# Performance work log

Hardware: AMD Instinct MI355X
Metric: run time of the kernel (lower is better)

Reference implementation:

```python
import jax, jax.numpy as jnp
import numpy as np

B, L, D, F, T = 32, 768, 256, 256, 3072
_EPS = 1e-5


def _layernorm(h, g, b):
    mu = jnp.mean(h, axis=-1, keepdims=True)
    var = jnp.var(h, axis=-1, keepdims=True)
    return (h - mu) * jax.lax.rsqrt(var + _EPS) * g + b


def _conv1d(h, w, b):
    # h: [B, L, Cin], w: [K, Cin, Cout] (HIO), padding=1 matches torch Conv1d(padding=1)
    return jax.lax.conv_general_dilated(h, w, (1,), [(1, 1)], dimension_numbers=('NHC', 'HIO', 'NHC')) + b


def setup_inputs() -> dict:
    key = jax.random.key(0)
    ks = jax.random.split(key, 6)
    return {
        'x': jax.random.normal(ks[0], (B, L, D), jnp.float32),
        'target': jax.random.randint(ks[1], (B, L), 0, 4, jnp.int32),
        'mel_max_length': T,
        'conv1_w': jax.random.normal(ks[2], (3, D, F), jnp.float32) * 0.05,
        'conv1_b': jnp.zeros((F,), jnp.float32),
        'ln1_g': jnp.ones((F,), jnp.float32),
        'ln1_b': jnp.zeros((F,), jnp.float32),
        'conv2_w': jax.random.normal(ks[3], (3, F, F), jnp.float32) * 0.05,
        'conv2_b': jnp.zeros((F,), jnp.float32),
        'ln2_g': jnp.ones((F,), jnp.float32),
        'ln2_b': jnp.zeros((F,), jnp.float32),
        'lin_w': jax.random.normal(ks[4], (F, 1), jnp.float32) * 0.05,
        'lin_b': jnp.zeros((1,), jnp.float32),
    }


def reference(x, target, mel_max_length, conv1_w, conv1_b, ln1_g, ln1_b,
              conv2_w, conv2_b, ln2_g, ln2_b, lin_w, lin_b):
    alpha = 1.0
    # DurationPredictor: conv -> relu -> LN -> conv -> relu -> LN -> linear (dropout=0)
    h = _layernorm(jax.nn.relu(_conv1d(x, conv1_w, conv1_b)), ln1_g, ln1_b)
    h = _layernorm(jax.nn.relu(_conv1d(h, conv2_w, conv2_b)), ln2_g, ln2_b)
    dp_out = (h @ lin_w + lin_b)[..., 0]                       # [B, L]
    durations = jnp.exp(dp_out) * alpha                        # [B, L] float
    # Training branch: durations come from target
    dpo = jnp.round(target.astype(jnp.float32) * alpha).astype(jnp.int32)  # [B, L]
    # LR: alignment @ x realized as cumulative-duration searchsorted + gather
    cum = jnp.cumsum(dpo, axis=1)                              # [B, L]
    t = jnp.arange(mel_max_length, dtype=jnp.int32)            # [T]
    idx = jax.vmap(lambda c: jnp.searchsorted(c, t, side='right'))(cum)  # [B, T]
    mask = (t[None, :] < cum[:, -1:]).astype(x.dtype)          # [B, T] zero past total frames
    out = jnp.take_along_axis(x, jnp.clip(idx, 0, x.shape[1] - 1)[:, :, None], axis=1)
    out = out * mask[:, :, None]                               # [B, T, D]
    return (out, dpo, durations)
```

## Files before the change

kernel.cpp:

```cpp
#include <hip/hip_runtime.h>
#include <hip/hip_bf16.h>
#include <math.h>

#define BB 32
#define LL 768
#define DD 256
#define FF 256
#define TT 3072
#define MT 32
#define OS 257

typedef __attribute__((ext_vector_type(8))) short bf16x8;
typedef __attribute__((ext_vector_type(4))) float f32x4;

__device__ inline unsigned short f2b(float f) {
    union { float f; unsigned u; } v; v.f = f;
    unsigned r = (v.u + 0x7FFF + ((v.u >> 16) & 1)) >> 16;
    return (unsigned short)r;
}

__global__ __launch_bounds__(256) void prep_w_kernel(
    const float* __restrict__ w1, const float* __restrict__ w2,
    unsigned short* __restrict__ wQ1, unsigned short* __restrict__ wQ2)
{
    const int layer = blockIdx.x / 24;
    const int s  = blockIdx.x % 24;
    const int kc = s >> 3, c8 = s & 7;
    const float* __restrict__ w = layer ? w2 : w1;
    unsigned short* __restrict__ o = (layer ? wQ2 : wQ1) + s * 8192 + threadIdx.x * 32;
    const int n = threadIdx.x;

    alignas(16) unsigned short tmp[32];
#pragma unroll
    for (int q = 0; q < 4; ++q)
#pragma unroll
        for (int j = 0; j < 8; ++j) {
            const int cin = c8 * 32 + q * 8 + j;
            tmp[q * 8 + j] = f2b(w[((size_t)(kc * 256 + cin)) * 256 + n]);
        }
#pragma unroll
    for (int i = 0; i < 4; ++i)
        *reinterpret_cast<uint4*>(o + i * 8) = *reinterpret_cast<const uint4*>(tmp + i * 8);
}

template <bool SECOND>
__global__ __launch_bounds__(256) void conv_mfma_kernel(
    const void* __restrict__ in_,
    const unsigned short* __restrict__ wQ,
    const float* __restrict__ cbias,
    const float* __restrict__ g,
    const float* __restrict__ be,
    const float* __restrict__ lin_w,
    const float* __restrict__ lin_b,
    unsigned short* __restrict__ out_h,
    float* __restrict__ out_dur)
{
    __shared__ union {
        unsigned short Af[48 * 64 * 8];
        float outs[MT * OS];
    } sm;
    __shared__ float red[4][MT][2];
    __shared__ float fin[MT][2];

    const int tid  = threadIdx.x;
    const int b    = blockIdx.x / (LL / MT);
    const int l0   = (blockIdx.x % (LL / MT)) * MT;
    const int wave = tid >> 6, lane = tid & 63;
    const int quad = lane >> 4, l16 = lane & 15;

    const int col = tid;
    const float biasv = cbias[col];
    const float gv  = g[col];
    const float bv  = be[col];
    const float lwv = SECOND ? lin_w[col] : 0.f;
    const float lbv = SECOND ? lin_b[0] : 0.f;

    for (int i = 0; i < 12; ++i) {
        const int combo = i * 4 + wave;
        const int mt = combo & 1;
        const int sc = combo >> 1;
        const int kc = sc >> 3, c8 = sc & 7;
        const int l  = l0 + mt * 16 + l16 + kc - 1;
        const int ch = c8 * 32 + quad * 8;
        bf16x8 val;
#pragma unroll
        for (int j = 0; j < 8; ++j) val[j] = 0;
        if (l >= 0 && l < LL) {
            if (!SECOND) {
                const float* p = (const float*)in_ + ((size_t)b * LL + l) * DD + ch;
                const float4 v0 = *reinterpret_cast<const float4*>(p);
                const float4 v1 = *reinterpret_cast<const float4*>(p + 4);
                val[0] = (short)f2b(v0.x); val[1] = (short)f2b(v0.y);
                val[2] = (short)f2b(v0.z); val[3] = (short)f2b(v0.w);
                val[4] = (short)f2b(v1.x); val[5] = (short)f2b(v1.y);
                val[6] = (short)f2b(v1.z); val[7] = (short)f2b(v1.w);
            } else {
                val = *reinterpret_cast<const bf16x8*>(
                    (const unsigned short*)in_ + ((size_t)b * LL + l) * DD + ch);
            }
        }
        *reinterpret_cast<bf16x8*>(&sm.Af[(combo * 64 + lane) * 8]) = val;
    }
    __syncthreads();

    const unsigned short* aptr = &sm.Af[lane * 8];
    const unsigned short* bptr = wQ + wave * 2048 + (l16 * 4 + quad) * 8;

    f32x4 acc[2][4] = {};
    bf16x8 a_c[2], b_c[4];
#pragma unroll
    for (int mt = 0; mt < 2; ++mt)
        a_c[mt] = *reinterpret_cast<const bf16x8*>(aptr + mt * 512);
#pragma unroll
    for (int nt = 0; nt < 4; ++nt)
        b_c[nt] = *reinterpret_cast<const bf16x8*>(bptr + nt * 512);

    for (int s = 0; s < 24; ++s) {
        bf16x8 a_n[2], b_n[4];
        if (s < 23) {
#pragma unroll
            for (int mt = 0; mt < 2; ++mt)
                a_n[mt] = *reinterpret_cast<const bf16x8*>(aptr + (s + 1) * 1024 + mt * 512);
#pragma unroll
            for (int nt = 0; nt < 4; ++nt)
                b_n[nt] = *reinterpret_cast<const bf16x8*>(bptr + (size_t)(s + 1) * 8192 + nt * 512);
        }
#pragma unroll
        for (int mt = 0; mt < 2; ++mt)
#pragma unroll
            for (int nt = 0; nt < 4; ++nt)
                acc[mt][nt] = __builtin_amdgcn_mfma_f32_16x16x32_bf16(
                    a_c[mt], b_c[nt], acc[mt][nt], 0, 0, 0);
        if (s < 23) {
#pragma unroll
            for (int mt = 0; mt < 2; ++mt) a_c[mt] = a_n[mt];
#pragma unroll
            for (int nt = 0; nt < 4; ++nt) b_c[nt] = b_n[nt];
        }
    }
    __syncthreads();

#pragma unroll
    for (int mt = 0; mt < 2; ++mt)
#pragma unroll
        for (int nt = 0; nt < 4; ++nt)
#pragma unroll
            for (int r = 0; r < 4; ++r)
                sm.outs[(mt * 16 + quad * 4 + r) * OS + wave * 64 + nt * 16 + l16] =
                    acc[mt][nt][r];
    __syncthreads();

    float vv[MT];
#pragma unroll
    for (int r = 0; r < MT; ++r)
        vv[r] = fmaxf(sm.outs[r * OS + col] + biasv, 0.f);

#pragma unroll
    for (int r = 0; r < MT; ++r) {
        float v = vv[r];
        float sum = v, sq = v * v;
        for (int off = 32; off > 0; off >>= 1) {
            sum += __shfl_down(sum, off, 64);
            sq  += __shfl_down(sq,  off, 64);
        }
        if (lane == 0) { red[wave][r][0] = sum; red[wave][r][1] = sq; }
    }
    __syncthreads();
    if (tid < MT) {
        const float sum = red[0][tid][0] + red[1][tid][0] + red[2][tid][0] + red[3][tid][0];
        const float sq  = red[0][tid][1] + red[1][tid][1] + red[2][tid][1] + red[3][tid][1];
        const float mu  = sum / FF;
        const float var = sq / FF - mu * mu;
        fin[tid][0] = mu;
        fin[tid][1] = rsqrtf(var + 1e-5f);
    }
    __syncthreads();

#pragma unroll
    for (int r = 0; r < MT; ++r) {
        const float v = (vv[r] - fin[r][0]) * fin[r][1] * gv + bv;
        if (!SECOND) {
            out_h[((size_t)b * LL + l0 + r) * FF + col] = f2b(v);
        } else {
            float p = v * lwv;
            for (int off = 32; off > 0; off >>= 1) p += __shfl_down(p, off, 64);
            if (lane == 0) red[wave][r][0] = p;
        }
    }
    if (SECOND) {
        __syncthreads();
        if (tid < MT) {
            const float dp = red[0][tid][0] + red[1][tid][0] + red[2][tid][0]
                           + red[3][tid][0] + lbv;
            out_dur[(size_t)b * LL + l0 + tid] = expf(dp);
        }
    }
}

__global__ __launch_bounds__(256) void scan_kernel(
    const int* __restrict__ target,
    float* __restrict__ out_dpo,
    int* __restrict__ idx_map)
{
    __shared__ int tsum[256];
    const int b = blockIdx.x, tid = threadIdx.x;

    const int l = 3 * tid;
    const int v0 = target[b * LL + l];
    const int v1 = target[b * LL + l + 1];
    const int v2 = target[b * LL + l + 2];
    out_dpo[b * LL + l]     = (float)v0;
    out_dpo[b * LL + l + 1] = (float)v1;
    out_dpo[b * LL + l + 2] = (float)v2;

    const int s0 = v0, s1 = v0 + v1, s2 = v0 + v1 + v2;
    tsum[tid] = s2;
    __syncthreads();
    for (int off = 1; off < 256; off <<= 1) {
        int x = (tid >= off) ? tsum[tid - off] : 0;
        __syncthreads();
        tsum[tid] += x;
        __syncthreads();
    }
    const int excl = tsum[tid] - s2;

    for (int t = tid; t < TT; t += 256) idx_map[b * TT + t] = -1;
    __syncthreads();

    const int c0 = excl + s0, c1 = excl + s1, c2 = excl + s2;
    for (int t = excl; t < c0 && t < TT; ++t) idx_map[b * TT + t] = l;
    for (int t = c0;   t < c1 && t < TT; ++t) idx_map[b * TT + t] = l + 1;
    for (int t = c1;   t < c2 && t < TT; ++t) idx_map[b * TT + t] = l + 2;
}

__global__ __launch_bounds__(256) void gather_kernel(
    const float* __restrict__ x,
    const int* __restrict__ idx_map,
    float* __restrict__ out)
{
    const int wv = threadIdx.x >> 6, lane = threadIdx.x & 63;
    const int row = blockIdx.x * 4 + wv;
    const int b = row / TT, t = row - b * TT;
    const int idx = idx_map[b * TT + t];
    float4 val = make_float4(0.f, 0.f, 0.f, 0.f);
    if (idx >= 0)
        val = reinterpret_cast<const float4*>(x)[(size_t)(b * LL + idx) * (DD / 4) + lane];
    reinterpret_cast<float4*>(out)[(size_t)row * (DD / 4) + lane] = val;
}

extern "C" void kernel_launch(void* const* d_in, const int* in_sizes, int n_in,
                              void* d_out, int out_size, void* d_ws, size_t ws_size,
                              hipStream_t stream)
{
    const float* x      = (const float*)d_in[0];
    const int*   target = (const int*)  d_in[1];
    const float* c1w = (const float*)d_in[3];
    const float* c1b = (const float*)d_in[4];
    const float* g1  = (const float*)d_in[5];
    const float* b1  = (const float*)d_in[6];
    const float* c2w = (const float*)d_in[7];
    const float* c2b = (const float*)d_in[8];
    const float* g2  = (const float*)d_in[9];
    const float* b2  = (const float*)d_in[10];
    const float* lw  = (const float*)d_in[11];
    const float* lb  = (const float*)d_in[12];

    float* out0    = (float*)d_out;
    float* out_dpo = out0 + (size_t)BB * TT * DD;
    float* out_dur = out_dpo + (size_t)BB * LL;

    char* ws = (char*)d_ws;
    unsigned short* wQ1 = (unsigned short*)ws;                 ws += (size_t)24 * 8192 * 2;
    unsigned short* wQ2 = (unsigned short*)ws;                 ws += (size_t)24 * 8192 * 2;
    unsigned short* h1b = (unsigned short*)ws;                 ws += (size_t)BB * LL * FF * 2;
    int* idx_map        = (int*)ws;

    prep_w_kernel<<<48, 256, 0, stream>>>(c1w, c2w, wQ1, wQ2);

    const int conv_grid = BB * (LL / MT);
    conv_mfma_kernel<false><<<conv_grid, 256, 0, stream>>>(
        x, wQ1, c1b, g1, b1, nullptr, nullptr, h1b, nullptr);
    conv_mfma_kernel<true><<<conv_grid, 256, 0, stream>>>(
        h1b, wQ2, c2b, g2, b2, lw, lb, nullptr, out_dur);

    scan_kernel<<<BB, 256, 0, stream>>>(target, out_dpo, idx_map);
    gather_kernel<<<BB * TT / 4, 256, 0, stream>>>(x, idx_map, out0);
}
```

Baseline: 235.3 us.

## Fuse both conv+LN layers into one kernel with halo recompute

Merges the two conv/ReLU/LayerNorm kernels into a single kernel per 32-row tile. Each block recomputes conv1 over a 2-row halo (48 rows) so conv2 can read h1 from shared memory, removing the global write and read of the bf16 intermediate and one launch. LayerNorm now reduces directly from MFMA accumulators via lane shuffles instead of staging through shared memory. The cost is about 50% extra conv1 MFMA work, and the B-operand prefetch double-buffering is dropped.

Result: faster. 209.0 us (-11.2%).

```diff
diff --git a/kernel.cpp b/kernel.cpp
--- a/kernel.cpp
+++ b/kernel.cpp
@@ -8,7 +8,8 @@
 #define FF 256
 #define TT 3072
 #define MT 32
-#define OS 257
+#define PAD 264
+#define A1R 50
 
 typedef __attribute__((ext_vector_type(8))) short bf16x8;
 typedef __attribute__((ext_vector_type(4))) float f32x4;
@@ -43,24 +44,22 @@
         *reinterpret_cast<uint4*>(o + i * 8) = *reinterpret_cast<const uint4*>(tmp + i * 8);
 }
 
-template <bool SECOND>
-__global__ __launch_bounds__(256) void conv_mfma_kernel(
-    const void* __restrict__ in_,
-    const unsigned short* __restrict__ wQ,
-    const float* __restrict__ cbias,
-    const float* __restrict__ g,
-    const float* __restrict__ be,
-    const float* __restrict__ lin_w,
-    const float* __restrict__ lin_b,
-    unsigned short* __restrict__ out_h,
+__global__ __launch_bounds__(256) void fused_dp_kernel(
+    const float* __restrict__ x,
+    const unsigned short* __restrict__ wQ1,
+    const unsigned short* __restrict__ wQ2,
+    const float* __restrict__ c1b, const float* __restrict__ g1, const float* __restrict__ b1,
+    const float* __restrict__ c2b, const float* __restrict__ g2, const float* __restrict__ b2,
+    const float* __restrict__ lw,  const float* __restrict__ lb,
     float* __restrict__ out_dur)
 {
     __shared__ union {
-        unsigned short Af[48 * 64 * 8];
-        float outs[MT * OS];
+        unsigned short A1[A1R * PAD];
+        unsigned short h2[34 * PAD];
     } sm;
-    __shared__ float red[4][MT][2];
-    __shared__ float fin[MT][2];
+    __shared__ float red[4][3][4][4][2];
+    __shared__ float redp[4][2][4][4];
+    __shared__ float fin[48][2];
 
     const int tid  = threadIdx.x;
     const int b    = blockIdx.x / (LL / MT);
@@ -68,132 +67,185 @@
     const int wave = tid >> 6, lane = tid & 63;
     const int quad = lane >> 4, l16 = lane & 15;
 
-    const int col = tid;
-    const float biasv = cbias[col];
-    const float gv  = g[col];
-    const float bv  = be[col];
-    const float lwv = SECOND ? lin_w[col] : 0.f;
-    const float lbv = SECOND ? lin_b[0] : 0.f;
-
-    for (int i = 0; i < 12; ++i) {
-        const int combo = i * 4 + wave;
-        const int mt = combo & 1;
-        const int sc = combo >> 1;
-        const int kc = sc >> 3, c8 = sc & 7;
-        const int l  = l0 + mt * 16 + l16 + kc - 1;
-        const int ch = c8 * 32 + quad * 8;
-        bf16x8 val;
-#pragma unroll
-        for (int j = 0; j < 8; ++j) val[j] = 0;
-        if (l >= 0 && l < LL) {
-            if (!SECOND) {
-                const float* p = (const float*)in_ + ((size_t)b * LL + l) * DD + ch;
-                const float4 v0 = *reinterpret_cast<const float4*>(p);
-                const float4 v1 = *reinterpret_cast<const float4*>(p + 4);
+    int   cols[4];
+    float c1bv[4], g1v[4], b1v[4], c2bv[4], g2v[4], b2v[4], lwv[4];
+#pragma unroll
+    for (int nt = 0; nt < 4; ++nt) {
+        const int c = wave * 64 + nt * 16 + l16;
+        cols[nt] = c;
+        c1bv[nt] = c1b[c]; g1v[nt] = g1[c]; b1v[nt] = b1[c];
+        c2bv[nt] = c2b[c]; g2v[nt] = g2[c]; b2v[nt] = b2[c];
+        lwv[nt]  = lw[c];
+    }
+    const float lbv = lb[0];
+
+    {
+        const int ch = (tid & 31) * 8;
+        const int rr = tid >> 5;
+        for (int p = 0; p < 7; ++p) {
+            const int ar = p * 8 + rr;
+            if (ar >= A1R) break;
+            const int l = l0 - 2 + ar;
+            bf16x8 val;
+#pragma unroll
+            for (int j = 0; j < 8; ++j) val[j] = 0;
+            if (l >= 0 && l < LL) {
+                const float* pp = x + ((size_t)b * LL + l) * DD + ch;
+                const float4 v0 = *reinterpret_cast<const float4*>(pp);
+                const float4 v1 = *reinterpret_cast<const float4*>(pp + 4);
                 val[0] = (short)f2b(v0.x); val[1] = (short)f2b(v0.y);
                 val[2] = (short)f2b(v0.z); val[3] = (short)f2b(v0.w);
                 val[4] = (short)f2b(v1.x); val[5] = (short)f2b(v1.y);
                 val[6] = (short)f2b(v1.z); val[7] = (short)f2b(v1.w);
-            } else {
-                val = *reinterpret_cast<const bf16x8*>(
-                    (const unsigned short*)in_ + ((size_t)b * LL + l) * DD + ch);
-            }
-        }
-        *reinterpret_cast<bf16x8*>(&sm.Af[(combo * 64 + lane) * 8]) = val;
-    }
-    __syncthreads();
-
-    const unsigned short* aptr = &sm.Af[lane * 8];
-    const unsigned short* bptr = wQ + wave * 2048 + (l16 * 4 + quad) * 8;
-
-    f32x4 acc[2][4] = {};
-    bf16x8 a_c[2], b_c[4];
-#pragma unroll
-    for (int mt = 0; mt < 2; ++mt)
-        a_c[mt] = *reinterpret_cast<const bf16x8*>(aptr + mt * 512);
-#pragma unroll
-    for (int nt = 0; nt < 4; ++nt)
-        b_c[nt] = *reinterpret_cast<const bf16x8*>(bptr + nt * 512);
-
+            }
+            *reinterpret_cast<bf16x8*>(&sm.A1[ar * PAD + ch]) = val;
+        }
+    }
+    __syncthreads();
+
+    f32x4 acc1[3][4] = {};
     for (int s = 0; s < 24; ++s) {
-        bf16x8 a_n[2], b_n[4];
-        if (s < 23) {
-#pragma unroll
-            for (int mt = 0; mt < 2; ++mt)
-                a_n[mt] = *reinterpret_cast<const bf16x8*>(aptr + (s + 1) * 1024 + mt * 512);
+        const int kc = s >> 3, c8 = s & 7;
+        bf16x8 a[3], bf[4];
+#pragma unroll
+        for (int mt = 0; mt < 3; ++mt)
+            a[mt] = *reinterpret_cast<const bf16x8*>(
+                &sm.A1[(16 * mt + l16 + kc) * PAD + c8 * 32 + quad * 8]);
+#pragma unroll
+        for (int nt = 0; nt < 4; ++nt)
+            bf[nt] = *reinterpret_cast<const bf16x8*>(
+                wQ1 + (size_t)s * 8192 + cols[nt] * 32 + quad * 8);
+#pragma unroll
+        for (int mt = 0; mt < 3; ++mt)
 #pragma unroll
             for (int nt = 0; nt < 4; ++nt)
-                b_n[nt] = *reinterpret_cast<const bf16x8*>(bptr + (size_t)(s + 1) * 8192 + nt * 512);
-        }
-#pragma unroll
-        for (int mt = 0; mt < 2; ++mt)
-#pragma unroll
-            for (int nt = 0; nt < 4; ++nt)
-                acc[mt][nt] = __builtin_amdgcn_mfma_f32_16x16x32_bf16(
-                    a_c[mt], b_c[nt], acc[mt][nt], 0, 0, 0);
-        if (s < 23) {
-#pragma unroll
-            for (int mt = 0; mt < 2; ++mt) a_c[mt] = a_n[mt];
-#pragma unroll
-            for (int nt = 0; nt < 4; ++nt) b_c[nt] = b_n[nt];
-        }
-    }
-    __syncthreads();
-
-#pragma unroll
-    for (int mt = 0; mt < 2; ++mt)
-#pragma unroll
-        for (int nt = 0; nt < 4; ++nt)
-#pragma unroll
-            for (int r = 0; r < 4; ++r)
-                sm.outs[(mt * 16 + quad * 4 + r) * OS + wave * 64 + nt * 16 + l16] =
-                    acc[mt][nt][r];
-    __syncthreads();
-
-    float vv[MT];
-#pragma unroll
-    for (int r = 0; r < MT; ++r)
-        vv[r] = fmaxf(sm.outs[r * OS + col] + biasv, 0.f);
-
-#pragma unroll
-    for (int r = 0; r < MT; ++r) {
-        float v = vv[r];
-        float sum = v, sq = v * v;
-        for (int off = 32; off > 0; off >>= 1) {
-            sum += __shfl_down(sum, off, 64);
-            sq  += __shfl_down(sq,  off, 64);
-        }
-        if (lane == 0) { red[wave][r][0] = sum; red[wave][r][1] = sq; }
-    }
-    __syncthreads();
-    if (tid < MT) {
-        const float sum = red[0][tid][0] + red[1][tid][0] + red[2][tid][0] + red[3][tid][0];
-        const float sq  = red[0][tid][1] + red[1][tid][1] + red[2][tid][1] + red[3][tid][1];
-        const float mu  = sum / FF;
-        const float var = sq / FF - mu * mu;
+                acc1[mt][nt] = __builtin_amdgcn_mfma_f32_16x16x32_bf16(
+                    a[mt], bf[nt], acc1[mt][nt], 0, 0, 0);
+    }
+    __syncthreads();
+
+#pragma unroll
+    for (int mt = 0; mt < 3; ++mt)
+#pragma unroll
+        for (int r = 0; r < 4; ++r) {
+            float s1 = 0.f, s2 = 0.f;
+#pragma unroll
+            for (int nt = 0; nt < 4; ++nt) {
+                const float v = fmaxf(acc1[mt][nt][r] + c1bv[nt], 0.f);
+                s1 += v; s2 += v * v;
+            }
+            for (int m = 1; m < 16; m <<= 1) {
+                s1 += __shfl_xor(s1, m, 64);
+                s2 += __shfl_xor(s2, m, 64);
+            }
+            if (l16 == 0) { red[wave][mt][quad][r][0] = s1; red[wave][mt][quad][r][1] = s2; }
+        }
+    __syncthreads();
+    if (tid < 48) {
+        const int mt = tid >> 4, q = (tid >> 2) & 3, r = tid & 3;
+        const float s1 = red[0][mt][q][r][0] + red[1][mt][q][r][0]
+                       + red[2][mt][q][r][0] + red[3][mt][q][r][0];
+        const float s2 = red[0][mt][q][r][1] + red[1][mt][q][r][1]
+                       + red[2][mt][q][r][1] + red[3][mt][q][r][1];
+        const float mu  = s1 * (1.f / 256.f);
+        const float var = s2 * (1.f / 256.f) - mu * mu;
         fin[tid][0] = mu;
         fin[tid][1] = rsqrtf(var + 1e-5f);
     }
     __syncthreads();
 
 #pragma unroll
-    for (int r = 0; r < MT; ++r) {
-        const float v = (vv[r] - fin[r][0]) * fin[r][1] * gv + bv;
-        if (!SECOND) {
-            out_h[((size_t)b * LL + l0 + r) * FF + col] = f2b(v);
-        } else {
-            float p = v * lwv;
-            for (int off = 32; off > 0; off >>= 1) p += __shfl_down(p, off, 64);
-            if (lane == 0) red[wave][r][0] = p;
-        }
-    }
-    if (SECOND) {
-        __syncthreads();
-        if (tid < MT) {
-            const float dp = red[0][tid][0] + red[1][tid][0] + red[2][tid][0]
-                           + red[3][tid][0] + lbv;
-            out_dur[(size_t)b * LL + l0 + tid] = expf(dp);
-        }
+    for (int mt = 0; mt < 3; ++mt)
+#pragma unroll
+        for (int r = 0; r < 4; ++r) {
+            const int rho = 16 * mt + quad * 4 + r;
+            if (rho < 34) {
+                const int gr = l0 - 1 + rho;
+                const float mu = fin[rho][0], rstd = fin[rho][1];
+#pragma unroll
+                for (int nt = 0; nt < 4; ++nt) {
+                    unsigned short hv = 0;
+                    if (gr >= 0 && gr < LL) {
+                        const float v = fmaxf(acc1[mt][nt][r] + c1bv[nt], 0.f);
+                        hv = f2b((v - mu) * rstd * g1v[nt] + b1v[nt]);
+                    }
+                    sm.h2[rho * PAD + cols[nt]] = hv;
+                }
+            }
+        }
+    __syncthreads();
+
+    f32x4 acc2[2][4] = {};
+    for (int s = 0; s < 24; ++s) {
+        const int kc = s >> 3, c8 = s & 7;
+        bf16x8 a[2], bf[4];
+#pragma unroll
+        for (int mt = 0; mt < 2; ++mt)
+            a[mt] = *reinterpret_cast<const bf16x8*>(
+                &sm.h2[(16 * mt + l16 + kc) * PAD + c8 * 32 + quad * 8]);
+#pragma unroll
+        for (int nt = 0; nt < 4; ++nt)
+            bf[nt] = *reinterpret_cast<const bf16x8*>(
+                wQ2 + (size_t)s * 8192 + cols[nt] * 32 + quad * 8);
+#pragma unroll
+        for (int mt = 0; mt < 2; ++mt)
+#pragma unroll
+            for (int nt = 0; nt < 4; ++nt)
+                acc2[mt][nt] = __builtin_amdgcn_mfma_f32_16x16x32_bf16(
+                    a[mt], bf[nt], acc2[mt][nt], 0, 0, 0);
+    }
+
+#pragma unroll
+    for (int mt = 0; mt < 2; ++mt)
+#pragma unroll
+        for (int r = 0; r < 4; ++r) {
+            float s1 = 0.f, s2 = 0.f;
+#pragma unroll
+            for (int nt = 0; nt < 4; ++nt) {
+                const float v = fmaxf(acc2[mt][nt][r] + c2bv[nt], 0.f);
+                s1 += v; s2 += v * v;
+            }
+            for (int m = 1; m < 16; m <<= 1) {
+                s1 += __shfl_xor(s1, m, 64);
+                s2 += __shfl_xor(s2, m, 64);
+            }
+            if (l16 == 0) { red[wave][mt][quad][r][0] = s1; red[wave][mt][quad][r][1] = s2; }
+        }
+    __syncthreads();
+    if (tid < 32) {
+        const int mt = tid >> 4, q = (tid >> 2) & 3, r = tid & 3;
+        const float s1 = red[0][mt][q][r][0] + red[1][mt][q][r][0]
+                       + red[2][mt][q][r][0] + red[3][mt][q][r][0];
+        const float s2 = red[0][mt][q][r][1] + red[1][mt][q][r][1]
+                       + red[2][mt][q][r][1] + red[3][mt][q][r][1];
+        const float mu  = s1 * (1.f / 256.f);
+        const float var = s2 * (1.f / 256.f) - mu * mu;
+        fin[tid][0] = mu;
+        fin[tid][1] = rsqrtf(var + 1e-5f);
+    }
+    __syncthreads();
+
+#pragma unroll
+    for (int mt = 0; mt < 2; ++mt)
+#pragma unroll
+        for (int r = 0; r < 4; ++r) {
+            const int rho = 16 * mt + quad * 4 + r;
+            const float mu = fin[rho][0], rstd = fin[rho][1];
+            float p = 0.f;
+#pragma unroll
+            for (int nt = 0; nt < 4; ++nt) {
+                const float v = fmaxf(acc2[mt][nt][r] + c2bv[nt], 0.f);
+                p += ((v - mu) * rstd * g2v[nt] + b2v[nt]) * lwv[nt];
+            }
+            for (int m = 1; m < 16; m <<= 1) p += __shfl_xor(p, m, 64);
+            if (l16 == 0) redp[wave][mt][quad][r] = p;
+        }
+    __syncthreads();
+    if (tid < 32) {
+        const int mt = tid >> 4, q = (tid >> 2) & 3, r = tid & 3;
+        const float dp = redp[0][mt][q][r] + redp[1][mt][q][r]
+                       + redp[2][mt][q][r] + redp[3][mt][q][r] + lbv;
+        out_dur[(size_t)b * LL + l0 + tid] = expf(dp);
     }
 }
 
@@ -217,9 +269,9 @@
     tsum[tid] = s2;
     __syncthreads();
     for (int off = 1; off < 256; off <<= 1) {
-        int x = (tid >= off) ? tsum[tid - off] : 0;
+        int xq = (tid >= off) ? tsum[tid - off] : 0;
         __syncthreads();
-        tsum[tid] += x;
+        tsum[tid] += xq;
         __syncthreads();
     }
     const int excl = tsum[tid] - s2;
@@ -272,16 +324,12 @@
     char* ws = (char*)d_ws;
     unsigned short* wQ1 = (unsigned short*)ws;                 ws += (size_t)24 * 8192 * 2;
     unsigned short* wQ2 = (unsigned short*)ws;                 ws += (size_t)24 * 8192 * 2;
-    unsigned short* h1b = (unsigned short*)ws;                 ws += (size_t)BB * LL * FF * 2;
     int* idx_map        = (int*)ws;
 
     prep_w_kernel<<<48, 256, 0, stream>>>(c1w, c2w, wQ1, wQ2);
 
-    const int conv_grid = BB * (LL / MT);
-    conv_mfma_kernel<false><<<conv_grid, 256, 0, stream>>>(
-        x, wQ1, c1b, g1, b1, nullptr, nullptr, h1b, nullptr);
-    conv_mfma_kernel<true><<<conv_grid, 256, 0, stream>>>(
-        h1b, wQ2, c2b, g2, b2, lw, lb, nullptr, out_dur);
+    fused_dp_kernel<<<BB * (LL / MT), 256, 0, stream>>>(
+        x, wQ1, wQ2, c1b, g1, b1, c2b, g2, b2, lw, lb, out_dur);
 
     scan_kernel<<<BB, 256, 0, stream>>>(target, out_dpo, idx_map);
     gather_kernel<<<BB * TT / 4, 256, 0, stream>>>(x, idx_map, out0);
```
